# Optimization experiments

Hardware: AMD Instinct MI355X
Metric: run time of the kernel (lower is better)

## Reference

```python
import jax, jax.numpy as jnp
import numpy as np
import math

B, H, S, D = 4, 16, 4096, 128

def setup_inputs() -> dict:
    key = jax.random.key(0)
    kq, kk, kv = jax.random.split(key, 3)
    q = jax.random.normal(kq, (B, H, S, D), dtype=jnp.float32)
    k = jax.random.normal(kk, (B, H, S, D), dtype=jnp.float32)
    v = jax.random.normal(kv, (B, H, S, D), dtype=jnp.float32)
    return {"q": q, "k": k, "v": v}

def reference(q, k, v):
    # Faithful to the torch module: score = (q^T @ k) / sqrt(n_heads)
    # q^T contracts over the SEQUENCE axis -> (B, H, D, D) feature-attention.
    n_heads = q.shape[1]
    scale = 1.0 / math.sqrt(n_heads)
    score = jnp.einsum('bhsd,bhse->bhde', q, k) * scale  # (B,H,D,D)
    score = jax.nn.softmax(score, axis=-1)
    # score @ v^T -> (B,H,D,S)
    out = jnp.einsum('bhde,bhse->bhds', score, v)
    return out
```

## Files before the change

### kernel.cpp

```cpp
#include <hip/hip_runtime.h>

#define BH 64
#define S_ 4096
#define D_ 128
#define SCALE 0.25f

typedef __attribute__((ext_vector_type(4))) short short4v;
typedef __attribute__((ext_vector_type(8))) short short8v;
typedef __attribute__((ext_vector_type(4))) float f32x4;

__device__ inline unsigned short f2bf(float x) {
  union { float f; unsigned u; } v; v.f = x;
  unsigned r = v.u + 0x7fff + ((v.u >> 16) & 1);
  return (unsigned short)(r >> 16);
}
__device__ inline short8v cat8(short4v a, short4v b) {
  short8v r;
  r[0] = a[0]; r[1] = a[1]; r[2] = a[2]; r[3] = a[3];
  r[4] = b[0]; r[5] = b[1]; r[6] = b[2]; r[7] = b[3];
  return r;
}
__device__ inline short4v tr16(unsigned addr) {
  short4v r;
  asm volatile("ds_read_b64_tr_b16 %0, %1" : "=v"(r) : "v"(addr));
  return r;
}
__device__ inline void cvt_pair(float x0, float x1, unsigned& hi, unsigned& lo) {
  unsigned u0 = __float_as_uint(x0), u1 = __float_as_uint(x1);
  unsigned m0 = u0 & 0xffff0000u, m1 = u1 & 0xffff0000u;
  hi = m1 | (u0 >> 16);
  float l0 = x0 - __uint_as_float(m0);
  float l1 = x1 - __uint_as_float(m1);
  lo = (__float_as_uint(l1) & 0xffff0000u) | (__float_as_uint(l0) >> 16);
}

#define TILE_SH 4352
#define TILE_U  2176
#define TILE_B  (TILE_SH * 2)
#define ROW_B 272
#define ROW_U 68

template <int NKS, bool ATOMIC>
__global__ __launch_bounds__(512, 2) void qk_mfma(const float* __restrict__ q,
                                                  const float* __restrict__ k,
                                                  float* __restrict__ part) {
  constexpr int schunk = S_ / NKS;
  constexpr int nsteps = schunk / 32;
  const int bh = blockIdx.x;
  const int ks = blockIdx.y;
  const float* qb = q + (size_t)bh * S_ * D_ + (size_t)ks * schunk * D_;
  const float* kb = k + (size_t)bh * S_ * D_ + (size_t)ks * schunk * D_;

  __shared__ alignas(16) short lds[4 * TILE_SH];
  unsigned* ldsU = (unsigned*)&lds[0];
  const unsigned base_u = (unsigned)(uintptr_t)&lds[0];

  const int tid = threadIdx.x;
  const int wv = tid >> 6, lane = tid & 63;
  const int wm = wv & 3;
  const int wn = wv >> 2;

  f32x4 acc[2][4];
#pragma unroll
  for (int a = 0; a < 2; ++a)
#pragma unroll
    for (int b = 0; b < 4; ++b) acc[a][b] = (f32x4){0.f, 0.f, 0.f, 0.f};

  const int lrow = ((lane >> 4) << 2) + ((lane & 15) >> 2);
  const unsigned trbase = base_u + (unsigned)lrow * ROW_B + (unsigned)(lane & 3) * 8;
  const unsigned aQ = trbase;
  const unsigned aK = trbase + 2u * TILE_B;

  const int r0 = tid >> 5;
  const int r1 = (tid + 512) >> 5;
  const int c4 = tid & 31;

  float4 qr[2], kr[2];
  auto load_step = [&](int st) {
    size_t o0 = (size_t)(st * 32 + r0) * D_ + c4 * 4;
    size_t o1 = (size_t)(st * 32 + r1) * D_ + c4 * 4;
    qr[0] = *(const float4*)(qb + o0);
    qr[1] = *(const float4*)(qb + o1);
    kr[0] = *(const float4*)(kb + o0);
    kr[1] = *(const float4*)(kb + o1);
  };
  auto cvt_store = [&]() {
#pragma unroll
    for (int i = 0; i < 2; ++i) {
      int row = i ? r1 : r0;
      unsigned* p = ldsU + row * ROW_U + c4 * 2;
      float4 xq = qr[i], xk = kr[i];
      unsigned h0, l0, h1, l1;
      cvt_pair(xq.x, xq.y, h0, l0);
      cvt_pair(xq.z, xq.w, h1, l1);
      *(uint2*)(p) = make_uint2(h0, h1);
      *(uint2*)(p + TILE_U) = make_uint2(l0, l1);
      cvt_pair(xk.x, xk.y, h0, l0);
      cvt_pair(xk.z, xk.w, h1, l1);
      *(uint2*)(p + 2 * TILE_U) = make_uint2(h0, h1);
      *(uint2*)(p + 3 * TILE_U) = make_uint2(l0, l1);
    }
  };

  load_step(0);
  cvt_store();
  if (nsteps > 1) load_step(1);
  asm volatile("s_waitcnt lgkmcnt(0)" ::: "memory");
  __builtin_amdgcn_s_barrier();
  __builtin_amdgcn_sched_barrier(0);

  for (int st = 0; st < nsteps; ++st) {
    short4v Bf[4][2][2];
#pragma unroll
    for (int b = 0; b < 4; ++b) {
      unsigned cb = (unsigned)(wn * 4 + b) * 32;
#pragma unroll
      for (int ver = 0; ver < 2; ++ver)
#pragma unroll
        for (int kh = 0; kh < 2; ++kh)
          Bf[b][ver][kh] = tr16(aK + ver * TILE_B + kh * (16 * ROW_B) + cb);
    }
    short4v Af[2][2][2];
#pragma unroll
    for (int a = 0; a < 2; ++a) {
      unsigned cb = (unsigned)(wm * 2 + a) * 32;
#pragma unroll
      for (int ver = 0; ver < 2; ++ver)
#pragma unroll
        for (int kh = 0; kh < 2; ++kh)
          Af[a][ver][kh] = tr16(aQ + ver * TILE_B + kh * (16 * ROW_B) + cb);
    }
    asm volatile("s_waitcnt lgkmcnt(0)" ::: "memory");
    __builtin_amdgcn_sched_barrier(0);
    __builtin_amdgcn_s_barrier();
    __builtin_amdgcn_sched_barrier(0);

    if (st + 1 < nsteps) cvt_store();
    if (st + 2 < nsteps) load_step(st + 2);

#pragma unroll
    for (int a = 0; a < 2; ++a) {
      short8v ah = cat8(Af[a][0][0], Af[a][0][1]);
      short8v al = cat8(Af[a][1][0], Af[a][1][1]);
#pragma unroll
      for (int b = 0; b < 4; ++b) {
        short8v bh_ = cat8(Bf[b][0][0], Bf[b][0][1]);
        short8v bl_ = cat8(Bf[b][1][0], Bf[b][1][1]);
        acc[a][b] = __builtin_amdgcn_mfma_f32_16x16x32_bf16(ah, bh_, acc[a][b], 0, 0, 0);
        acc[a][b] = __builtin_amdgcn_mfma_f32_16x16x32_bf16(ah, bl_, acc[a][b], 0, 0, 0);
        acc[a][b] = __builtin_amdgcn_mfma_f32_16x16x32_bf16(al, bh_, acc[a][b], 0, 0, 0);
      }
    }
    asm volatile("s_waitcnt lgkmcnt(0)" ::: "memory");
    __builtin_amdgcn_sched_barrier(0);
    __builtin_amdgcn_s_barrier();
    __builtin_amdgcn_sched_barrier(0);
  }

  if (!ATOMIC) {
    float* dst = part + ((size_t)ks * BH + bh) * D_ * D_;
#pragma unroll
    for (int a = 0; a < 2; ++a)
#pragma unroll
      for (int b = 0; b < 4; ++b) {
        int e = (wn * 4 + b) * 16 + (lane & 15);
#pragma unroll
        for (int r = 0; r < 4; ++r) {
          int d = (wm * 2 + a) * 16 + ((lane >> 4) << 2) + r;
          dst[(size_t)d * D_ + e] = acc[a][b][r] * SCALE;
        }
      }
  } else {
    float* dst = part + (size_t)bh * D_ * D_;
#pragma unroll
    for (int a = 0; a < 2; ++a)
#pragma unroll
      for (int b = 0; b < 4; ++b) {
        int e = (wn * 4 + b) * 16 + (lane & 15);
#pragma unroll
        for (int r = 0; r < 4; ++r) {
          int d = (wm * 2 + a) * 16 + ((lane >> 4) << 2) + r;
          atomicAdd(&dst[(size_t)d * D_ + e], acc[a][b][r] * SCALE);
        }
      }
  }
}

template <int NKS>
__global__ __launch_bounds__(256) void softmax_k(const float* __restrict__ part,
                                                 short* __restrict__ Pg) {
  const int bh = blockIdx.x;
  const int wv = threadIdx.x >> 6, lane = threadIdx.x & 63;
  const size_t kstride = (size_t)BH * D_ * D_;
  const float* base = part + (size_t)bh * D_ * D_;
  short* dst = Pg + (size_t)bh * D_ * D_;
#pragma unroll
  for (int i = 0; i < 8; ++i) {
    int d = blockIdx.y * 32 + wv * 8 + i;
    float v0 = 0.f, v1 = 0.f;
    for (int ks2 = 0; ks2 < NKS; ++ks2) {
      const float* row = base + ks2 * kstride + (size_t)d * D_;
      v0 += row[lane];
      v1 += row[lane + 64];
    }
    float m = fmaxf(v0, v1);
#pragma unroll
    for (int off = 32; off; off >>= 1) m = fmaxf(m, __shfl_xor(m, off, 64));
    float e0 = __expf(v0 - m), e1 = __expf(v1 - m);
    float s = e0 + e1;
#pragma unroll
    for (int off = 32; off; off >>= 1) s += __shfl_xor(s, off, 64);
    float inv = 1.f / s;
    dst[(size_t)d * D_ + lane] = (short)f2bf(e0 * inv);
    dst[(size_t)d * D_ + lane + 64] = (short)f2bf(e1 * inv);
  }
}

__global__ __launch_bounds__(256) void pv_mfma(const short* __restrict__ Pg,
                                               const float* __restrict__ v,
                                               float* __restrict__ out) {
  const int bh = blockIdx.x;
  const int s0 = blockIdx.y * 128;
  const float* vb = v + (size_t)bh * S_ * D_;
  __shared__ alignas(16) short P_lds[128 * 136];
  __shared__ alignas(16) short V_lds[128 * 36];
  const int tid = threadIdx.x;
  const int wv = tid >> 6, lane = tid & 63;

  const short* Pb = Pg + (size_t)bh * D_ * D_;
#pragma unroll
  for (int i = 0; i < 8; ++i) {
    int idx8 = tid + i * 256;
    int row = idx8 >> 4, c8 = idx8 & 15;
    short8v val = *(const short8v*)(Pb + row * 128 + c8 * 8);
    *(short8v*)(P_lds + row * 136 + c8 * 8) = val;
  }

  f32x4 acc[8][2];
#pragma unroll
  for (int i = 0; i < 8; ++i)
#pragma unroll
    for (int j = 0; j < 2; ++j) acc[i][j] = (f32x4){0.f, 0.f, 0.f, 0.f};

#pragma unroll
  for (int es = 0; es < 4; ++es) {
    __syncthreads();
#pragma unroll
    for (int i = 0; i < 4; ++i) {
      int idx4 = tid + i * 256;
      int s = idx4 >> 3, c4 = idx4 & 7;
      float4 x = *(const float4*)(vb + (size_t)(s0 + s) * D_ + es * 32 + c4 * 4);
      short4v h;
      h[0] = (short)f2bf(x.x); h[1] = (short)f2bf(x.y);
      h[2] = (short)f2bf(x.z); h[3] = (short)f2bf(x.w);
      *(short4v*)(V_lds + s * 36 + c4 * 4) = h;
    }
    __syncthreads();

    short8v a[8];
#pragma unroll
    for (int mt = 0; mt < 8; ++mt) {
      int d = mt * 16 + (lane & 15);
      const short* pr = P_lds + d * 136 + es * 32 + ((lane >> 4) << 2);
      a[mt] = cat8(*(const short4v*)pr, *(const short4v*)(pr + 16));
    }
#pragma unroll
    for (int nl = 0; nl < 2; ++nl) {
      int srow = (wv * 2 + nl) * 16 + (lane & 15);
      const short* vr = V_lds + srow * 36 + ((lane >> 4) << 2);
      short8v b = cat8(*(const short4v*)vr, *(const short4v*)(vr + 16));
#pragma unroll
      for (int mt = 0; mt < 8; ++mt)
        acc[mt][nl] = __builtin_amdgcn_mfma_f32_16x16x32_bf16(a[mt], b, acc[mt][nl], 0, 0, 0);
    }
  }

  float* ob = out + (size_t)bh * D_ * S_ + s0;
#pragma unroll
  for (int mt = 0; mt < 8; ++mt)
#pragma unroll
    for (int nl = 0; nl < 2; ++nl) {
      int sc = (wv * 2 + nl) * 16 + (lane & 15);
#pragma unroll
      for (int r = 0; r < 4; ++r) {
        int d = mt * 16 + ((lane >> 4) << 2) + r;
        ob[(size_t)d * S_ + sc] = acc[mt][nl][r];
      }
    }
}

extern "C" void kernel_launch(void* const* d_in, const int* in_sizes, int n_in,
                              void* d_out, int out_size, void* d_ws,
                              size_t ws_size, hipStream_t stream) {
  const float* q = (const float*)d_in[0];
  const float* k = (const float*)d_in[1];
  const float* v = (const float*)d_in[2];
  float* out = (float*)d_out;
  char* ws = (char*)d_ws;

  const size_t PART1 = (size_t)BH * D_ * D_ * sizeof(float);
  const size_t PSZ = (size_t)BH * D_ * D_ * sizeof(short);

  if (ws_size >= 8 * PART1 + PSZ) {
    float* part = (float*)ws;
    short* Pg = (short*)(ws + 8 * PART1);
    qk_mfma<8, false><<<dim3(BH, 8), 512, 0, stream>>>(q, k, part);
    softmax_k<8><<<dim3(BH, 4), 256, 0, stream>>>(part, Pg);
    pv_mfma<<<dim3(BH, 32), 256, 0, stream>>>(Pg, v, out);
  } else {
    float* part = (float*)ws;
    short* Pg = (short*)(ws + PART1);
    hipMemsetAsync(ws, 0, PART1, stream);
    qk_mfma<16, true><<<dim3(BH, 16), 512, 0, stream>>>(q, k, part);
    softmax_k<1><<<dim3(BH, 4), 256, 0, stream>>>(part, Pg);
    pv_mfma<<<dim3(BH, 32), 256, 0, stream>>>(Pg, v, out);
  }
}
```

Measured before the change: 151.4 us.

## Double-buffer LDS tiles to drop one barrier per step in QK kernel

Doubles the LDS staging area into two buffers and alternates between them each step. Fragments are read from one buffer while the next step's converted tile is written into the other, so only one barrier per step remains instead of two. The cost is doubled LDS use per block (about 69 KB), which may lower occupancy below the two blocks per CU the launch bounds target.

After: 151.7 us. About the same (+0.2%).

```diff
diff --git a/kernel.cpp b/kernel.cpp
--- a/kernel.cpp
+++ b/kernel.cpp
@@ -37,6 +37,8 @@
 #define TILE_SH 4352
 #define TILE_U  2176
 #define TILE_B  (TILE_SH * 2)
+#define BUF_SH  (4 * TILE_SH)
+#define BUF_B   (4 * TILE_B)
 #define ROW_B 272
 #define ROW_U 68
 
@@ -46,13 +48,15 @@
                                                   float* __restrict__ part) {
   constexpr int schunk = S_ / NKS;
   constexpr int nsteps = schunk / 32;
+  static_assert(nsteps % 2 == 0, "nsteps must be even (buffer pairing)");
   const int bh = blockIdx.x;
   const int ks = blockIdx.y;
   const float* qb = q + (size_t)bh * S_ * D_ + (size_t)ks * schunk * D_;
   const float* kb = k + (size_t)bh * S_ * D_ + (size_t)ks * schunk * D_;
 
-  __shared__ alignas(16) short lds[4 * TILE_SH];
-  unsigned* ldsU = (unsigned*)&lds[0];
+  __shared__ alignas(16) short lds[2 * BUF_SH];
+  unsigned* ldsU0 = (unsigned*)&lds[0];
+  unsigned* ldsU1 = (unsigned*)&lds[BUF_SH];
   const unsigned base_u = (unsigned)(uintptr_t)&lds[0];
 
   const int tid = threadIdx.x;
@@ -68,8 +72,10 @@
 
   const int lrow = ((lane >> 4) << 2) + ((lane & 15) >> 2);
   const unsigned trbase = base_u + (unsigned)lrow * ROW_B + (unsigned)(lane & 3) * 8;
-  const unsigned aQ = trbase;
-  const unsigned aK = trbase + 2u * TILE_B;
+  const unsigned aQ0 = trbase;
+  const unsigned aK0 = trbase + 2u * TILE_B;
+  const unsigned aQ1 = aQ0 + BUF_B;
+  const unsigned aK1 = aK0 + BUF_B;
 
   const int r0 = tid >> 5;
   const int r1 = (tid + 512) >> 5;
@@ -84,11 +90,11 @@
     kr[0] = *(const float4*)(kb + o0);
     kr[1] = *(const float4*)(kb + o1);
   };
-  auto cvt_store = [&]() {
+  auto cvt_store = [&](unsigned* bufU) {
 #pragma unroll
     for (int i = 0; i < 2; ++i) {
       int row = i ? r1 : r0;
-      unsigned* p = ldsU + row * ROW_U + c4 * 2;
+      unsigned* p = bufU + row * ROW_U + c4 * 2;
       float4 xq = qr[i], xk = kr[i];
       unsigned h0, l0, h1, l1;
       cvt_pair(xq.x, xq.y, h0, l0);
@@ -102,14 +108,7 @@
     }
   };
 
-  load_step(0);
-  cvt_store();
-  if (nsteps > 1) load_step(1);
-  asm volatile("s_waitcnt lgkmcnt(0)" ::: "memory");
-  __builtin_amdgcn_s_barrier();
-  __builtin_amdgcn_sched_barrier(0);
-
-  for (int st = 0; st < nsteps; ++st) {
+  auto iter = [&](int st, unsigned aQb, unsigned aKb, unsigned* stageU) {
     short4v Bf[4][2][2];
 #pragma unroll
     for (int b = 0; b < 4; ++b) {
@@ -118,7 +117,7 @@
       for (int ver = 0; ver < 2; ++ver)
 #pragma unroll
         for (int kh = 0; kh < 2; ++kh)
-          Bf[b][ver][kh] = tr16(aK + ver * TILE_B + kh * (16 * ROW_B) + cb);
+          Bf[b][ver][kh] = tr16(aKb + ver * TILE_B + kh * (16 * ROW_B) + cb);
     }
     short4v Af[2][2][2];
 #pragma unroll
@@ -128,16 +127,12 @@
       for (int ver = 0; ver < 2; ++ver)
 #pragma unroll
         for (int kh = 0; kh < 2; ++kh)
-          Af[a][ver][kh] = tr16(aQ + ver * TILE_B + kh * (16 * ROW_B) + cb);
-    }
+          Af[a][ver][kh] = tr16(aQb + ver * TILE_B + kh * (16 * ROW_B) + cb);
+    }
+    if (st + 1 < nsteps) cvt_store(stageU);
+    if (st + 2 < nsteps) load_step(st + 2);
     asm volatile("s_waitcnt lgkmcnt(0)" ::: "memory");
     __builtin_amdgcn_sched_barrier(0);
-    __builtin_amdgcn_s_barrier();
-    __builtin_amdgcn_sched_barrier(0);
-
-    if (st + 1 < nsteps) cvt_store();
-    if (st + 2 < nsteps) load_step(st + 2);
-
 #pragma unroll
     for (int a = 0; a < 2; ++a) {
       short8v ah = cat8(Af[a][0][0], Af[a][0][1]);
@@ -151,10 +146,18 @@
         acc[a][b] = __builtin_amdgcn_mfma_f32_16x16x32_bf16(al, bh_, acc[a][b], 0, 0, 0);
       }
     }
-    asm volatile("s_waitcnt lgkmcnt(0)" ::: "memory");
-    __builtin_amdgcn_sched_barrier(0);
     __builtin_amdgcn_s_barrier();
-    __builtin_amdgcn_sched_barrier(0);
+  };
+
+  load_step(0);
+  cvt_store(ldsU0);
+  if (nsteps > 1) load_step(1);
+  asm volatile("s_waitcnt lgkmcnt(0)" ::: "memory");
+  __builtin_amdgcn_s_barrier();
+
+  for (int st = 0; st < nsteps; st += 2) {
+    iter(st, aQ0, aK0, ldsU1);
+    iter(st + 1, aQ1, aK1, ldsU0);
   }
 
   if (!ATOMIC) {
```
